# Optimization experiments

Measured on AMD Instinct MI355X. Metric: run time of the kernel, lower is better.

Reference implementation:

```python
import jax, jax.numpy as jnp
from jax import lax
import numpy as np

EPS = 1e-5
SLOPE = 0.01  # torch LeakyReLU default


def sub_conv(feats, nbr, W):
    """Sparse gather-GEMM-scatter conv.
    feats: [M, Ci] input-site features; nbr: [N, K] indices into feats rows
    (rulebook); W: [K, Ci, Co]. Returns [N, Co].
    Loop over the K kernel taps (fixed, small) via scan to avoid
    materializing the [N, K, Ci] gathered tensor."""
    N = nbr.shape[0]
    Co = W.shape[2]
    def step(acc, kW):
        idx, Wk = kW
        return acc + feats[idx] @ Wk, None
    acc0 = jnp.zeros((N, Co), feats.dtype)
    acc, _ = lax.scan(step, acc0, (nbr.T, W))
    return acc


def batch_norm(f, g, b):
    # nn.BatchNorm1d forward (training mode): stats over the voxel axis
    mean = f.mean(axis=0)
    var = f.var(axis=0)
    return (f - mean) * lax.rsqrt(var + EPS) * g + b


def setup_inputs() -> dict:
    key = jax.random.key(0)
    ks = jax.random.split(key, 20)
    N_low, N_up = 120000, 240000
    Ci, Co = 128, 64

    x_feats = jax.random.normal(ks[0], (N_low, Ci), jnp.float32)
    skip_feats = jax.random.normal(ks[1], (N_up, Co), jnp.float32)

    # rulebooks: random neighbor indices; center tap = identity (submanifold)
    nbr1 = jax.random.randint(ks[2], (N_low, 27), 0, N_low).at[:, 13].set(jnp.arange(N_low))
    nbr_up = jax.random.randint(ks[3], (N_up, 27), 0, N_low)  # inverse conv: N_up outputs from N_low inputs
    nbr2 = jax.random.randint(ks[4], (N_up, 9), 0, N_up).at[:, 4].set(jnp.arange(N_up))
    nbr3 = jax.random.randint(ks[5], (N_up, 9), 0, N_up).at[:, 4].set(jnp.arange(N_up))
    nbr4 = jax.random.randint(ks[6], (N_up, 27), 0, N_up).at[:, 13].set(jnp.arange(N_up))

    def w(k, shape, fan_in):
        return jax.random.normal(k, shape, jnp.float32) * (1.0 / np.sqrt(fan_in))

    W1 = w(ks[7], (27, Ci, Co), 27 * Ci)
    Wup = w(ks[8], (27, Co, Co), 27 * Co)
    W2 = w(ks[9], (9, Co, Co), 9 * Co)
    W3 = w(ks[10], (9, Co, Co), 9 * Co)
    W4 = w(ks[11], (27, Co, Co), 27 * Co)

    ones = jnp.ones((Co,), jnp.float32)
    zeros = jnp.zeros((Co,), jnp.float32)
    return dict(x_feats=x_feats, skip_feats=skip_feats,
                nbr1=nbr1, nbr_up=nbr_up, nbr2=nbr2, nbr3=nbr3, nbr4=nbr4,
                W1=W1, Wup=Wup, W2=W2, W3=W3, W4=W4,
                g1=ones, b1=zeros, g2=ones, b2=zeros,
                g3=ones, b3=zeros, g4=ones, b4=zeros)


def reference(x_feats, skip_feats, nbr1, nbr_up, nbr2, nbr3, nbr4,
              W1, Wup, W2, W3, W4, g1, b1, g2, b2, g3, b3, g4, b4):
    up = sub_conv(x_feats, nbr1, W1)               # [N_low, Co]
    up = batch_norm(jax.nn.leaky_relu(up, SLOPE), g1, b1)
    up = sub_conv(up, nbr_up, Wup)                 # inverse conv -> [N_up, Co]
    up = up + skip_feats                           # residual add
    up = sub_conv(up, nbr2, W2)                    # 1x3x3
    up = batch_norm(jax.nn.leaky_relu(up, SLOPE), g2, b2)
    up = sub_conv(up, nbr3, W3)                    # 3x1x3
    up = batch_norm(jax.nn.leaky_relu(up, SLOPE), g3, b3)
    up = sub_conv(up, nbr4, W4)                    # 3x3x3
    up = batch_norm(jax.nn.leaky_relu(up, SLOPE), g4, b4)
    return up
```

## Files before the change

### kernel.cpp

```cpp
#include <hip/hip_runtime.h>
#include <hip/hip_bf16.h>


typedef __attribute__((ext_vector_type(8))) short bf16x8;
typedef __attribute__((ext_vector_type(4))) float f32x4;

__device__ __forceinline__ short f2bf(float f) {
    union { float f; unsigned u; } v; v.f = f;
    unsigned r = v.u + 0x7fffu + ((v.u >> 16) & 1u);
    return (short)(r >> 16);
}
__device__ __forceinline__ float bf2f(short s) {
    union { unsigned u; float f; } v;
    v.u = ((unsigned)(unsigned short)s) << 16;
    return v.f;
}

__device__ __forceinline__ void gload16(const void* g, void* l) {
    __builtin_amdgcn_global_load_lds(
        (const __attribute__((address_space(1))) char*)g,
        (__attribute__((address_space(3))) char*)l, 16, 0, 0);
}

__global__ void cast_kernel(const float* __restrict__ in, short* __restrict__ out, int total) {
    int e = (blockIdx.x * blockDim.x + threadIdx.x) * 8;
    if (e >= total) return;
    bf16x8 r;
#pragma unroll
    for (int j = 0; j < 8; ++j) r[j] = f2bf(in[e + j]);
    *(bf16x8*)(out + e) = r;
}

template <int H>
__global__ void pack_w_kernel(const float* __restrict__ w, short* __restrict__ wp,
                              const float* __restrict__ ss, int total) {
    int t = blockIdx.x * blockDim.x + threadIdx.x;
    if (t >= total) return;
    int ci2 = t & 63;
    int co = (t >> 6) & 63;
    int tap = t >> 12;
    int k = tap / H, half = tap % H;
    int ci = half * 64 + ci2;
    float v = w[(k * (64 * H) + ci) * 64 + co];
    if (ss) v *= ss[ci];
    wp[t] = f2bf(v);
}

__global__ void bias_kernel(const float* __restrict__ w, const float* __restrict__ ss,
                            int CI, float* __restrict__ bias) {
    int k = blockIdx.x;
    int co = threadIdx.x;
    float acc = 0.f;
    for (int ci = 0; ci < CI; ++ci)
        acc += ss[64 + ci] * w[(k * CI + ci) * 64 + co];
    atomicAdd(&bias[co], acc);
}

template <int KTAB, int H>
struct ConvCtx {
    static constexpr int KT2 = KTAB * H;
    static constexpr int P = (KT2 + 1) / 2;
    const char* finb;
    const char* wpb;
    const int* snbr;
    short* abufw;
    short (*wbufs)[8192];
    int row0, row1;
    int lane, lr, lg, wid;
    int CIB;
};

template <int t, int KTAB, int H>
__device__ __forceinline__ void issue_gather(const ConvCtx<KTAB, H>& c) {
    constexpr int k = (H == 2) ? (t >> 1) : t;
    constexpr int halfoff = (H == 2) ? ((t & 1) * 128) : 0;
    int i0 = c.snbr[c.row0 * KTAB + k];
    int i1 = c.snbr[c.row1 * KTAB + k];
    const char* b0 = c.finb + (size_t)i0 * c.CIB + halfoff + c.lg * 16;
    const char* b1 = c.finb + (size_t)i1 * c.CIB + halfoff + c.lg * 16;
    short* d = c.abufw + (t & 1) * 2048;
    gload16(b0,      d);
    gload16(b0 + 64, d + 512);
    gload16(b1,      d + 1024);
    gload16(b1 + 64, d + 1536);
}

template <int p, int KTAB, int H>
__device__ __forceinline__ void issue_w(const ConvCtx<KTAB, H>& c, int wlaneoff) {
    const char* s = c.wpb + (size_t)p * 16384 + c.wid * 4096 + wlaneoff;
    short* d = c.wbufs[p & 1] + c.wid * 2048;
    gload16(s,        d);
    gload16(s + 1024, d + 512);
    gload16(s + 2048, d + 1024);
    gload16(s + 3072, d + 1536);
}

template <int t, int KTAB, int H>
__device__ __forceinline__ void tap_step(const ConvCtx<KTAB, H>& c, int wlaneoff,
                                         int woff0, int woff1, f32x4 (&acc)[2][4]) {
    constexpr int KT2 = ConvCtx<KTAB, H>::KT2;
    constexpr int P = ConvCtx<KTAB, H>::P;
    constexpr int NW = ((t & 1) == 0)
        ? (4 * ((t + 1 <= KT2 - 1) ? 1 : 0))
        : (4 * ((t + 1 <= KT2 - 1) ? 1 : 0) + 4 * (((t + 1) / 2 <= P - 1) ? 1 : 0));
    asm volatile("s_waitcnt vmcnt(%0)" :: "i"(NW) : "memory");
    if constexpr ((t & 1) == 0) {
        __builtin_amdgcn_s_barrier();
        if constexpr (t / 2 + 1 <= P - 1)
            issue_w<t / 2 + 1>(c, wlaneoff);
    }
    const short* ab = c.abufw + (t & 1) * 2048 + c.lane * 8;
    bf16x8 a00 = *(const bf16x8*)(ab);
    bf16x8 a01 = *(const bf16x8*)(ab + 512);
    bf16x8 a10 = *(const bf16x8*)(ab + 1024);
    bf16x8 a11 = *(const bf16x8*)(ab + 1536);
    const char* wt = (const char*)(c.wbufs[(t >> 1) & 1] + (t & 1) * 4096) + c.lr * 128;
    bf16x8 w0[4], w1[4];
#pragma unroll
    for (int ct = 0; ct < 4; ++ct) {
        w0[ct] = *(const bf16x8*)(wt + ct * 2048 + woff0);
        w1[ct] = *(const bf16x8*)(wt + ct * 2048 + woff1);
    }
    asm volatile("s_waitcnt lgkmcnt(0)" ::: "memory");
    if constexpr (t + 2 <= KT2 - 1)
        issue_gather<t + 2>(c);
#pragma unroll
    for (int ct = 0; ct < 4; ++ct) {
        acc[0][ct] = __builtin_amdgcn_mfma_f32_16x16x32_bf16(a00, w0[ct], acc[0][ct], 0, 0, 0);
        acc[1][ct] = __builtin_amdgcn_mfma_f32_16x16x32_bf16(a10, w0[ct], acc[1][ct], 0, 0, 0);
        acc[0][ct] = __builtin_amdgcn_mfma_f32_16x16x32_bf16(a01, w1[ct], acc[0][ct], 0, 0, 0);
        acc[1][ct] = __builtin_amdgcn_mfma_f32_16x16x32_bf16(a11, w1[ct], acc[1][ct], 0, 0, 0);
    }
}

template <int t, int KTAB, int H>
__device__ __forceinline__ void run_taps(const ConvCtx<KTAB, H>& c, int wlaneoff,
                                         int woff0, int woff1, f32x4 (&acc)[2][4]) {
    tap_step<t>(c, wlaneoff, woff0, woff1, acc);
    if constexpr (t + 1 < ConvCtx<KTAB, H>::KT2)
        run_taps<t + 1>(c, wlaneoff, woff0, woff1, acc);
}

template <int KTAB, int H, int MODE, bool HAS_BIAS>
__global__ __launch_bounds__(256, 2) void conv_kernel(
    const short* __restrict__ fin, const int* __restrict__ nbr,
    const short* __restrict__ wp, const float* __restrict__ bias,
    const float* __restrict__ skip, short* __restrict__ fout,
    int N, float* __restrict__ sums)
{
    constexpr int KT2 = KTAB * H;
    __shared__ int snbr[128 * KTAB];
    __shared__ __align__(16) short abuf[4][2][2048];
    __shared__ __align__(16) short wbufs[2][8192];
    __shared__ float sred[128];

    const int tid = threadIdx.x;
    const int lane = tid & 63;
    const int wid = tid >> 6;
    const int lr = lane & 15;
    const int lg = lane >> 4;
    const int rowbase = blockIdx.x * 128;
    const int nrows = (N - rowbase < 128) ? (N - rowbase) : 128;

    for (int i = tid; i < nrows * KTAB; i += 256)
        snbr[i] = __builtin_nontemporal_load(&nbr[(size_t)rowbase * KTAB + i]);
    if (MODE == 0 && tid < 128) sred[tid] = 0.f;
    __syncthreads();

    const int rb0 = wid * 32 + lr;
    const int rb1 = wid * 32 + 16 + lr;

    ConvCtx<KTAB, H> c;
    c.finb = (const char*)fin;
    c.wpb = (const char*)wp;
    c.snbr = snbr;
    c.abufw = &abuf[wid][0][0];
    c.wbufs = wbufs;
    c.row0 = (rb0 < nrows ? rb0 : nrows - 1);
    c.row1 = (rb1 < nrows ? rb1 : nrows - 1);
    c.lane = lane; c.lr = lr; c.lg = lg; c.wid = wid;
    c.CIB = 64 * H * 2;

    const int wlaneoff = (lane >> 3) * 128 + (((lane & 7) * 16) ^ ((lane >> 3) << 4));
    const int wsw = (lr & 7) << 4;
    const int woff0 = (lg * 16) ^ wsw;
    const int woff1 = (lg * 16 + 64) ^ wsw;

    f32x4 acc[2][4];
#pragma unroll
    for (int q = 0; q < 2; ++q)
#pragma unroll
        for (int cct = 0; cct < 4; ++cct) acc[q][cct] = (f32x4)(0.f);

    issue_w<0>(c, wlaneoff);
    issue_gather<0>(c);
    issue_gather<1>(c);
    run_taps<0>(c, wlaneoff, woff0, woff1, acc);

    float bia[4] = {0.f, 0.f, 0.f, 0.f};
    if (HAS_BIAS) {
#pragma unroll
        for (int ct = 0; ct < 4; ++ct) bia[ct] = bias[ct * 16 + lr];
    }
    float bsum[4] = {0.f, 0.f, 0.f, 0.f};
    float bsq[4] = {0.f, 0.f, 0.f, 0.f};
    const int wrow = wid * 32;
#pragma unroll
    for (int q = 0; q < 2; ++q) {
#pragma unroll
        for (int reg = 0; reg < 4; ++reg) {
            const int r = rowbase + wrow + q * 16 + lg * 4 + reg;
            const bool valid = r < N;
#pragma unroll
            for (int ct = 0; ct < 4; ++ct) {
                float v = acc[q][ct][reg];
                if (HAS_BIAS) v += bia[ct];
                if (MODE == 0) {
                    v = v > 0.f ? v : 0.01f * v;
                    if (valid) {
                        fout[(size_t)r * 64 + ct * 16 + lr] = f2bf(v);
                        bsum[ct] += v;
                        bsq[ct] += v * v;
                    }
                } else {
                    if (valid) {
                        v += skip[(size_t)r * 64 + ct * 16 + lr];
                        fout[(size_t)r * 64 + ct * 16 + lr] = f2bf(v);
                    }
                }
            }
        }
    }

    if (MODE == 0) {
#pragma unroll
        for (int ct = 0; ct < 4; ++ct) {
            float s = bsum[ct], q = bsq[ct];
            s += __shfl_xor(s, 16); s += __shfl_xor(s, 32);
            q += __shfl_xor(q, 16); q += __shfl_xor(q, 32);
            if (lg == 0) {
                atomicAdd(&sred[ct * 16 + lr], s);
                atomicAdd(&sred[64 + ct * 16 + lr], q);
            }
        }
        __syncthreads();
        if (tid < 128) atomicAdd(&sums[tid], sred[tid]);
    }
}

__global__ void finalize_kernel(const float* __restrict__ sums, const float* __restrict__ g,
                                const float* __restrict__ b, float invN, float* __restrict__ ss) {
    int c = threadIdx.x;
    float mean = sums[c] * invN;
    float var = sums[64 + c] * invN - mean * mean;
    float sc = g[c] * rsqrtf(var + 1e-5f);
    ss[c] = sc;
    ss[64 + c] = b[c] - mean * sc;
}

__global__ void final_norm_kernel(const short* __restrict__ in, const float* __restrict__ ss,
                                  float* __restrict__ out, int total) {
    int e = (blockIdx.x * blockDim.x + threadIdx.x) * 8;
    if (e >= total) return;
    bf16x8 v = *(const bf16x8*)(in + e);
    int c0 = e & 63;
#pragma unroll
    for (int j = 0; j < 8; ++j)
        out[e + j] = bf2f(v[j]) * ss[c0 + j] + ss[64 + c0 + j];
}

extern "C" void kernel_launch(void* const* d_in, const int* in_sizes, int n_in,
                              void* d_out, int out_size, void* d_ws, size_t ws_size,
                              hipStream_t stream) {
    const float* x    = (const float*)d_in[0];
    const float* skip = (const float*)d_in[1];
    const int* nbr1 = (const int*)d_in[2];
    const int* nbrU = (const int*)d_in[3];
    const int* nbr2 = (const int*)d_in[4];
    const int* nbr3 = (const int*)d_in[5];
    const int* nbr4 = (const int*)d_in[6];
    const float* W1 = (const float*)d_in[7];
    const float* WU = (const float*)d_in[8];
    const float* W2 = (const float*)d_in[9];
    const float* W3 = (const float*)d_in[10];
    const float* W4 = (const float*)d_in[11];
    const float* g1 = (const float*)d_in[12]; const float* b1 = (const float*)d_in[13];
    const float* g2 = (const float*)d_in[14]; const float* b2 = (const float*)d_in[15];
    const float* g3 = (const float*)d_in[16]; const float* b3 = (const float*)d_in[17];
    const float* g4 = (const float*)d_in[18]; const float* b4 = (const float*)d_in[19];

    const int Nl = in_sizes[0] / 128;
    const int Nu = in_sizes[1] / 64;

    char* ws = (char*)d_ws;
    size_t off = 0;
    auto alloc = [&](size_t bytes) -> char* {
        char* p = ws + off;
        off += (bytes + 255) & ~(size_t)255;
        return p;
    };
    const size_t fbig = (size_t)Nu * 64 * 2;
    const size_t xb = (size_t)Nl * 128 * 2;
    short* A = (short*)alloc(xb > fbig ? xb : fbig);
    short* B = (short*)alloc(fbig);
    short* C = (short*)alloc(fbig);
    short* Wp1 = (short*)alloc((size_t)54 * 8192);
    short* WpU = (short*)alloc((size_t)28 * 8192);
    short* Wp2 = (short*)alloc((size_t)10 * 8192);
    short* Wp3 = (short*)alloc((size_t)10 * 8192);
    short* Wp4 = (short*)alloc((size_t)28 * 8192);
    float* sums = (float*)alloc((512 + 192) * sizeof(float));
    float* biasU = sums + 512;
    float* bias3 = sums + 576;
    float* bias4 = sums + 640;
    float* ss = (float*)alloc(4 * 128 * sizeof(float));

    hipMemsetAsync(sums, 0, (512 + 192) * sizeof(float), stream);

    cast_kernel<<<(Nl * 128 / 8 + 255) / 256, 256, 0, stream>>>(x, A, Nl * 128);
    pack_w_kernel<2><<<(54 * 4096 + 255) / 256, 256, 0, stream>>>(W1, Wp1, nullptr, 54 * 4096);
    pack_w_kernel<1><<<(9 * 4096 + 255) / 256, 256, 0, stream>>>(W2, Wp2, nullptr, 9 * 4096);

    const int gl = (Nl + 127) / 128;
    const int gu = (Nu + 127) / 128;

    conv_kernel<27, 2, 0, false><<<gl, 256, 0, stream>>>(A, nbr1, Wp1, nullptr, nullptr, B, Nl, sums + 0);
    finalize_kernel<<<1, 64, 0, stream>>>(sums + 0, g1, b1, 1.f / Nl, ss + 0);
    pack_w_kernel<1><<<(27 * 4096 + 255) / 256, 256, 0, stream>>>(WU, WpU, ss + 0, 27 * 4096);
    bias_kernel<<<27, 64, 0, stream>>>(WU, ss + 0, 64, biasU);

    conv_kernel<27, 1, 1, true><<<gu, 256, 0, stream>>>(B, nbrU, WpU, biasU, skip, C, Nu, nullptr);

    conv_kernel<9, 1, 0, false><<<gu, 256, 0, stream>>>(C, nbr2, Wp2, nullptr, nullptr, A, Nu, sums + 128);
    finalize_kernel<<<1, 64, 0, stream>>>(sums + 128, g2, b2, 1.f / Nu, ss + 128);
    pack_w_kernel<1><<<(9 * 4096 + 255) / 256, 256, 0, stream>>>(W3, Wp3, ss + 128, 9 * 4096);
    bias_kernel<<<9, 64, 0, stream>>>(W3, ss + 128, 64, bias3);

    conv_kernel<9, 1, 0, true><<<gu, 256, 0, stream>>>(A, nbr3, Wp3, bias3, nullptr, B, Nu, sums + 256);
    finalize_kernel<<<1, 64, 0, stream>>>(sums + 256, g3, b3, 1.f / Nu, ss + 256);
    pack_w_kernel<1><<<(27 * 4096 + 255) / 256, 256, 0, stream>>>(W4, Wp4, ss + 256, 27 * 4096);
    bias_kernel<<<27, 64, 0, stream>>>(W4, ss + 256, 64, bias4);

    conv_kernel<27, 1, 0, true><<<gu, 256, 0, stream>>>(B, nbr4, Wp4, bias4, nullptr, C, Nu, sums + 384);
    finalize_kernel<<<1, 64, 0, stream>>>(sums + 384, g4, b4, 1.f / Nu, ss + 384);

    final_norm_kernel<<<(Nu * 64 / 8 + 255) / 256, 256, 0, stream>>>(C, ss + 384, (float*)d_out, Nu * 64);
}
```

Before: 791.9 us.

## Deepen conv gather and weight prefetch pipeline to six A slots and four W slots

The conv kernel's software pipeline changes from double-buffered gathers and paired-tap weight loads to a six-slot per-wave gather ring and a four-slot per-tap weight ring. Gathers are issued six taps ahead and weights three taps ahead, with a barrier every tap and sched_barriers to pin instruction order. The aim is to hide more global-gather latency. In exchange, shared memory rises to roughly 130KB and launch bounds drop to one block per CU, which reduces occupancy and adds a barrier on every tap.

```diff
diff --git a/kernel.cpp b/kernel.cpp
--- a/kernel.cpp
+++ b/kernel.cpp
@@ -57,101 +57,93 @@
 }
 
 template <int KTAB, int H>
-struct ConvCtx {
+struct CC {
     static constexpr int KT2 = KTAB * H;
-    static constexpr int P = (KT2 + 1) / 2;
     const char* finb;
     const char* wpb;
     const int* snbr;
-    short* abufw;
-    short (*wbufs)[8192];
+    char* aslot;
+    char* wbuf;
     int row0, row1;
-    int lane, lr, lg, wid;
+    int lg16;
+    int wsrc;
+    int wdst;
     int CIB;
 };
 
-template <int t, int KTAB, int H>
-__device__ __forceinline__ void issue_gather(const ConvCtx<KTAB, H>& c) {
-    constexpr int k = (H == 2) ? (t >> 1) : t;
-    constexpr int halfoff = (H == 2) ? ((t & 1) * 128) : 0;
+template <int tw, int KTAB, int H>
+__device__ __forceinline__ void issue_w(const CC<KTAB, H>& c) {
+    const char* s = c.wpb + (size_t)tw * 8192 + c.wsrc;
+    char* d = c.wbuf + (tw & 3) * 8192 + c.wdst;
+    gload16(s, d);
+    gload16(s + 1024, d + 1024);
+}
+
+template <int ta, int KTAB, int H>
+__device__ __forceinline__ void issue_a(const CC<KTAB, H>& c) {
+    constexpr int k = (H == 2) ? (ta >> 1) : ta;
+    constexpr int hoff = (H == 2) ? ((ta & 1) * 128) : 0;
     int i0 = c.snbr[c.row0 * KTAB + k];
     int i1 = c.snbr[c.row1 * KTAB + k];
-    const char* b0 = c.finb + (size_t)i0 * c.CIB + halfoff + c.lg * 16;
-    const char* b1 = c.finb + (size_t)i1 * c.CIB + halfoff + c.lg * 16;
-    short* d = c.abufw + (t & 1) * 2048;
+    const char* b0 = c.finb + (size_t)i0 * c.CIB + hoff + c.lg16;
+    const char* b1 = c.finb + (size_t)i1 * c.CIB + hoff + c.lg16;
+    char* d = c.aslot + (ta % 6) * 4096;
     gload16(b0,      d);
-    gload16(b0 + 64, d + 512);
-    gload16(b1,      d + 1024);
-    gload16(b1 + 64, d + 1536);
-}
-
-template <int p, int KTAB, int H>
-__device__ __forceinline__ void issue_w(const ConvCtx<KTAB, H>& c, int wlaneoff) {
-    const char* s = c.wpb + (size_t)p * 16384 + c.wid * 4096 + wlaneoff;
-    short* d = c.wbufs[p & 1] + c.wid * 2048;
-    gload16(s,        d);
-    gload16(s + 1024, d + 512);
-    gload16(s + 2048, d + 1024);
-    gload16(s + 3072, d + 1536);
+    gload16(b0 + 64, d + 1024);
+    gload16(b1,      d + 2048);
+    gload16(b1 + 64, d + 3072);
 }
 
 template <int t, int KTAB, int H>
-__device__ __forceinline__ void tap_step(const ConvCtx<KTAB, H>& c, int wlaneoff,
-                                         int woff0, int woff1, f32x4 (&acc)[2][4]) {
-    constexpr int KT2 = ConvCtx<KTAB, H>::KT2;
-    constexpr int P = ConvCtx<KTAB, H>::P;
-    constexpr int NW = ((t & 1) == 0)
-        ? (4 * ((t + 1 <= KT2 - 1) ? 1 : 0))
-        : (4 * ((t + 1 <= KT2 - 1) ? 1 : 0) + 4 * (((t + 1) / 2 <= P - 1) ? 1 : 0));
+__device__ __forceinline__ void body(const CC<KTAB, H>& c, int lane, int lr,
+                                     int wk0, int wk1, f32x4 (&acc)[2][4]) {
+    constexpr int KT2 = CC<KTAB, H>::KT2;
+    constexpr int NW =
+        (t == 0) ? 20 : (t == 1) ? 22 : (t == 2) ? 24 :
+        4 * (((t + 3 < KT2) ? 1 : 0) + ((t + 4 < KT2) ? 1 : 0) + ((t + 5 < KT2) ? 1 : 0)) +
+        2 * (((t + 1 < KT2) ? 1 : 0) + ((t + 2 < KT2) ? 1 : 0));
     asm volatile("s_waitcnt vmcnt(%0)" :: "i"(NW) : "memory");
-    if constexpr ((t & 1) == 0) {
-        __builtin_amdgcn_s_barrier();
-        if constexpr (t / 2 + 1 <= P - 1)
-            issue_w<t / 2 + 1>(c, wlaneoff);
-    }
-    const short* ab = c.abufw + (t & 1) * 2048 + c.lane * 8;
-    bf16x8 a00 = *(const bf16x8*)(ab);
-    bf16x8 a01 = *(const bf16x8*)(ab + 512);
-    bf16x8 a10 = *(const bf16x8*)(ab + 1024);
-    bf16x8 a11 = *(const bf16x8*)(ab + 1536);
-    const char* wt = (const char*)(c.wbufs[(t >> 1) & 1] + (t & 1) * 4096) + c.lr * 128;
+    __builtin_amdgcn_sched_barrier(0);
+    __builtin_amdgcn_s_barrier();
+    __builtin_amdgcn_sched_barrier(0);
+    if constexpr (t + 3 < KT2) issue_w<t + 3>(c);
+
+    const char* as = c.aslot + (t % 6) * 4096 + lane * 16;
+    bf16x8 a0 = *(const bf16x8*)(as);
+    bf16x8 a1 = *(const bf16x8*)(as + 1024);
+    bf16x8 a2 = *(const bf16x8*)(as + 2048);
+    bf16x8 a3 = *(const bf16x8*)(as + 3072);
+    const char* wsb = c.wbuf + (t & 3) * 8192 + lr * 128;
     bf16x8 w0[4], w1[4];
 #pragma unroll
     for (int ct = 0; ct < 4; ++ct) {
-        w0[ct] = *(const bf16x8*)(wt + ct * 2048 + woff0);
-        w1[ct] = *(const bf16x8*)(wt + ct * 2048 + woff1);
+        w0[ct] = *(const bf16x8*)(wsb + ct * 2048 + wk0);
+        w1[ct] = *(const bf16x8*)(wsb + ct * 2048 + wk1);
     }
     asm volatile("s_waitcnt lgkmcnt(0)" ::: "memory");
-    if constexpr (t + 2 <= KT2 - 1)
-        issue_gather<t + 2>(c);
+    __builtin_amdgcn_sched_barrier(0);
+    if constexpr (t + 6 < KT2) issue_a<t + 6>(c);
+
 #pragma unroll
     for (int ct = 0; ct < 4; ++ct) {
-        acc[0][ct] = __builtin_amdgcn_mfma_f32_16x16x32_bf16(a00, w0[ct], acc[0][ct], 0, 0, 0);
-        acc[1][ct] = __builtin_amdgcn_mfma_f32_16x16x32_bf16(a10, w0[ct], acc[1][ct], 0, 0, 0);
-        acc[0][ct] = __builtin_amdgcn_mfma_f32_16x16x32_bf16(a01, w1[ct], acc[0][ct], 0, 0, 0);
-        acc[1][ct] = __builtin_amdgcn_mfma_f32_16x16x32_bf16(a11, w1[ct], acc[1][ct], 0, 0, 0);
-    }
-}
-
-template <int t, int KTAB, int H>
-__device__ __forceinline__ void run_taps(const ConvCtx<KTAB, H>& c, int wlaneoff,
-                                         int woff0, int woff1, f32x4 (&acc)[2][4]) {
-    tap_step<t>(c, wlaneoff, woff0, woff1, acc);
-    if constexpr (t + 1 < ConvCtx<KTAB, H>::KT2)
-        run_taps<t + 1>(c, wlaneoff, woff0, woff1, acc);
+        acc[0][ct] = __builtin_amdgcn_mfma_f32_16x16x32_bf16(a0, w0[ct], acc[0][ct], 0, 0, 0);
+        acc[0][ct] = __builtin_amdgcn_mfma_f32_16x16x32_bf16(a1, w1[ct], acc[0][ct], 0, 0, 0);
+        acc[1][ct] = __builtin_amdgcn_mfma_f32_16x16x32_bf16(a2, w0[ct], acc[1][ct], 0, 0, 0);
+        acc[1][ct] = __builtin_amdgcn_mfma_f32_16x16x32_bf16(a3, w1[ct], acc[1][ct], 0, 0, 0);
+    }
+    if constexpr (t + 1 < KT2) body<t + 1>(c, lane, lr, wk0, wk1, acc);
 }
 
 template <int KTAB, int H, int MODE, bool HAS_BIAS>
-__global__ __launch_bounds__(256, 2) void conv_kernel(
+__global__ __launch_bounds__(256, 1) void conv_kernel(
     const short* __restrict__ fin, const int* __restrict__ nbr,
     const short* __restrict__ wp, const float* __restrict__ bias,
     const float* __restrict__ skip, short* __restrict__ fout,
     int N, float* __restrict__ sums)
 {
-    constexpr int KT2 = KTAB * H;
     __shared__ int snbr[128 * KTAB];
-    __shared__ __align__(16) short abuf[4][2][2048];
-    __shared__ __align__(16) short wbufs[2][8192];
+    __shared__ __align__(16) char wbuf[4 * 8192];
+    __shared__ __align__(16) char abuf[4][6 * 4096];
     __shared__ float sred[128];
 
     const int tid = threadIdx.x;
@@ -170,32 +162,32 @@
     const int rb0 = wid * 32 + lr;
     const int rb1 = wid * 32 + 16 + lr;
 
-    ConvCtx<KTAB, H> c;
+    CC<KTAB, H> c;
     c.finb = (const char*)fin;
     c.wpb = (const char*)wp;
     c.snbr = snbr;
-    c.abufw = &abuf[wid][0][0];
-    c.wbufs = wbufs;
+    c.aslot = &abuf[wid][0];
+    c.wbuf = wbuf;
     c.row0 = (rb0 < nrows ? rb0 : nrows - 1);
     c.row1 = (rb1 < nrows ? rb1 : nrows - 1);
-    c.lane = lane; c.lr = lr; c.lg = lg; c.wid = wid;
+    c.lg16 = lg * 16;
+    c.wsrc = wid * 2048 + (lane >> 3) * 128 + (((lane & 7) ^ ((lane >> 3) & 7)) << 4);
+    c.wdst = wid * 2048;
     c.CIB = 64 * H * 2;
 
-    const int wlaneoff = (lane >> 3) * 128 + (((lane & 7) * 16) ^ ((lane >> 3) << 4));
-    const int wsw = (lr & 7) << 4;
-    const int woff0 = (lg * 16) ^ wsw;
-    const int woff1 = (lg * 16 + 64) ^ wsw;
+    const int wk0 = ((lg) ^ (lr & 7)) << 4;
+    const int wk1 = ((4 + lg) ^ (lr & 7)) << 4;
 
     f32x4 acc[2][4];
 #pragma unroll
     for (int q = 0; q < 2; ++q)
 #pragma unroll
-        for (int cct = 0; cct < 4; ++cct) acc[q][cct] = (f32x4)(0.f);
-
-    issue_w<0>(c, wlaneoff);
-    issue_gather<0>(c);
-    issue_gather<1>(c);
-    run_taps<0>(c, wlaneoff, woff0, woff1, acc);
+        for (int ct = 0; ct < 4; ++ct) acc[q][ct] = (f32x4)(0.f);
+
+    issue_w<0>(c); issue_w<1>(c); issue_w<2>(c);
+    issue_a<0>(c); issue_a<1>(c); issue_a<2>(c);
+    issue_a<3>(c); issue_a<4>(c); issue_a<5>(c);
+    body<0>(c, lane, lr, wk0, wk1, acc);
 
     float bia[4] = {0.f, 0.f, 0.f, 0.f};
     if (HAS_BIAS) {
@@ -305,10 +297,10 @@
     short* B = (short*)alloc(fbig);
     short* C = (short*)alloc(fbig);
     short* Wp1 = (short*)alloc((size_t)54 * 8192);
-    short* WpU = (short*)alloc((size_t)28 * 8192);
-    short* Wp2 = (short*)alloc((size_t)10 * 8192);
-    short* Wp3 = (short*)alloc((size_t)10 * 8192);
-    short* Wp4 = (short*)alloc((size_t)28 * 8192);
+    short* WpU = (short*)alloc((size_t)27 * 8192);
+    short* Wp2 = (short*)alloc((size_t)9 * 8192);
+    short* Wp3 = (short*)alloc((size_t)9 * 8192);
+    short* Wp4 = (short*)alloc((size_t)27 * 8192);
     float* sums = (float*)alloc((512 + 192) * sizeof(float));
     float* biasU = sums + 512;
     float* bias3 = sums + 576;
```

Measured after the change: 1.072 ms (median of 4 runs). +35.4%, slower.
